# Performance work log

Measured on AMD Instinct MI355X. Metric: run time of the kernel, lower is better.

## Reference

```python
import jax, jax.numpy as jnp
import numpy as np

N, E = 4096, 131072
IN_DIM, HID, OUT_DIM = 128, 64, 128
H1 = 4                       # gat1 heads
D_MODEL = HID * H1           # 256
NHEAD = 4
D_FF = 2048


def setup_inputs() -> dict:
    key = jax.random.key(0)
    ks = jax.random.split(key, 16)
    def w(k, shape, scale=0.05):
        return jax.random.normal(k, shape, dtype=jnp.float32) * scale
    return {
        "x": jax.random.normal(ks[0], (N, IN_DIM), dtype=jnp.float32),
        "edge_index": jax.random.randint(ks[1], (2, E), 0, N, dtype=jnp.int32),
        "gat1_w": w(ks[2], (H1 * HID, IN_DIM)),
        "gat1_asrc": w(ks[3], (H1, HID)),
        "gat1_adst": w(ks[4], (H1, HID)),
        "gat1_b": jnp.zeros((H1 * HID,), jnp.float32),
        "in_proj_w": w(ks[5], (3 * D_MODEL, D_MODEL)),
        "in_proj_b": jnp.zeros((3 * D_MODEL,), jnp.float32),
        "out_proj_w": w(ks[6], (D_MODEL, D_MODEL)),
        "out_proj_b": jnp.zeros((D_MODEL,), jnp.float32),
        "lin1_w": w(ks[7], (D_FF, D_MODEL)),
        "lin1_b": jnp.zeros((D_FF,), jnp.float32),
        "lin2_w": w(ks[8], (D_MODEL, D_FF)),
        "lin2_b": jnp.zeros((D_MODEL,), jnp.float32),
        "ln1_g": jnp.ones((D_MODEL,), jnp.float32),
        "ln1_b": jnp.zeros((D_MODEL,), jnp.float32),
        "ln2_g": jnp.ones((D_MODEL,), jnp.float32),
        "ln2_b": jnp.zeros((D_MODEL,), jnp.float32),
        "gat2_w": w(ks[9], (OUT_DIM, D_MODEL)),
        "gat2_asrc": w(ks[10], (1, OUT_DIM)),
        "gat2_adst": w(ks[11], (1, OUT_DIM)),
        "gat2_b": jnp.zeros((OUT_DIM,), jnp.float32),
    }


def _add_self_loops(ei, n):
    loops = jnp.arange(n, dtype=ei.dtype)
    return jnp.concatenate([ei, jnp.stack([loops, loops])], axis=1)


def _segment_softmax(logits, seg, n):
    # numerically stable softmax over edges grouped by destination node
    m = jax.ops.segment_max(logits, seg, num_segments=n)
    m = jnp.where(jnp.isfinite(m), m, 0.0)
    e = jnp.exp(logits - m[seg])
    s = jax.ops.segment_sum(e, seg, num_segments=n)
    return e / (s[seg] + 1e-16)


def _gat(x, ei, W, asrc, adst, b, heads, out_ch):
    n = x.shape[0]
    h = (x @ W.T).reshape(n, heads, out_ch)          # [N,H,C]
    al_s = jnp.einsum('nhc,hc->nh', h, asrc)
    al_d = jnp.einsum('nhc,hc->nh', h, adst)
    src, dst = ei[0], ei[1]
    logits = jax.nn.leaky_relu(al_s[src] + al_d[dst], 0.2)   # [E,H]
    alpha = _segment_softmax(logits, dst, n)
    out = jax.ops.segment_sum(h[src] * alpha[:, :, None], dst, num_segments=n)
    return out.reshape(n, heads * out_ch) + b


def _ln(x, g, b):
    mu = x.mean(-1, keepdims=True)
    v = x.var(-1, keepdims=True)
    return (x - mu) / jnp.sqrt(v + 1e-5) * g + b


def _forward(x, edge_index, gat1_w, gat1_asrc, gat1_adst, gat1_b,
             in_proj_w, in_proj_b, out_proj_w, out_proj_b,
             lin1_w, lin1_b, lin2_w, lin2_b, ln1_g, ln1_b, ln2_g, ln2_b,
             gat2_w, gat2_asrc, gat2_adst, gat2_b):
    n = x.shape[0]
    ei = _add_self_loops(edge_index, n)
    h = jax.nn.elu(_gat(x, ei, gat1_w, gat1_asrc, gat1_adst, gat1_b, H1, HID))  # [N, 256]
    # TransformerEncoderLayer (post-norm, relu, no dropout in eval)
    hd = D_MODEL // NHEAD
    qkv = h @ in_proj_w.T + in_proj_b
    q, k, v = jnp.split(qkv, 3, axis=-1)
    q = q.reshape(n, NHEAD, hd)
    k = k.reshape(n, NHEAD, hd)
    v = v.reshape(n, NHEAD, hd)
    scores = jnp.einsum('qhd,khd->hqk', q, k) / jnp.sqrt(jnp.float32(hd))
    attn = jax.nn.softmax(scores, axis=-1)
    o = jnp.einsum('hqk,khd->qhd', attn, v).reshape(n, D_MODEL)
    o = o @ out_proj_w.T + out_proj_b
    h = _ln(h + o, ln1_g, ln1_b)
    ff = jax.nn.relu(h @ lin1_w.T + lin1_b) @ lin2_w.T + lin2_b
    h = _ln(h + ff, ln2_g, ln2_b)
    return _gat(h, ei, gat2_w, gat2_asrc, gat2_adst, gat2_b, 1, OUT_DIM)


def reference(x, edge_index, gat1_w, gat1_asrc, gat1_adst, gat1_b,
              in_proj_w, in_proj_b, out_proj_w, out_proj_b,
              lin1_w, lin1_b, lin2_w, lin2_b, ln1_g, ln1_b, ln2_g, ln2_b,
              gat2_w, gat2_asrc, gat2_adst, gat2_b):
    return _forward(x, edge_index, gat1_w, gat1_asrc, gat1_adst, gat1_b,
                    in_proj_w, in_proj_b, out_proj_w, out_proj_b,
                    lin1_w, lin1_b, lin2_w, lin2_b, ln1_g, ln1_b, ln2_g, ln2_b,
                    gat2_w, gat2_asrc, gat2_adst, gat2_b)
```

## Files before the change

kernel.cpp:

```cpp
#include <hip/hip_runtime.h>
#include <hip/hip_bf16.h>
#include <math.h>

#define NN 4096
#define NE 131072
#define EE (NE + NN)

typedef unsigned short u16;
typedef short s8v __attribute__((ext_vector_type(8)));
typedef float f4v __attribute__((ext_vector_type(4)));
typedef float f16v __attribute__((ext_vector_type(16)));

__device__ inline u16 f2b(float f) {
  __hip_bfloat16 h = __float2bfloat16(f);
  return __builtin_bit_cast(u16, h);
}
__device__ inline float b2f(u16 v) {
  unsigned int u = ((unsigned int)v) << 16;
  return __builtin_bit_cast(float, u);
}

__global__ void k_count(const int* __restrict__ ei, int* __restrict__ deg) {
  int e = blockIdx.x * 256 + threadIdx.x;
  if (e >= EE) return;
  int dst = (e < NE) ? ei[NE + e] : (e - NE);
  atomicAdd(&deg[dst], 1);
}

__global__ __launch_bounds__(1024) void k_scan(const int* __restrict__ deg, int* __restrict__ rowptr) {
  __shared__ int lds[1024];
  int t = threadIdx.x;
  int v0 = deg[t*4+0], v1 = deg[t*4+1], v2 = deg[t*4+2], v3 = deg[t*4+3];
  int s1 = v0+v1, s2 = s1+v2, s3 = s2+v3;
  lds[t] = s3;
  __syncthreads();
  for (int off = 1; off < 1024; off <<= 1) {
    int add = (t >= off) ? lds[t-off] : 0;
    __syncthreads();
    lds[t] += add;
    __syncthreads();
  }
  int base = lds[t] - s3;
  rowptr[t*4+1] = base + v0;
  rowptr[t*4+2] = base + s1;
  rowptr[t*4+3] = base + s2;
  rowptr[t*4+4] = base + s3;
  if (t == 0) rowptr[0] = 0;
}

__global__ void k_scatter(const int* __restrict__ ei, const int* __restrict__ rowptr,
                          int* __restrict__ cursor, int* __restrict__ csr_src) {
  int e = blockIdx.x * 256 + threadIdx.x;
  if (e >= EE) return;
  int src, dst;
  if (e < NE) { src = ei[e]; dst = ei[NE + e]; }
  else { src = e - NE; dst = src; }
  int pos = rowptr[dst] + atomicAdd(&cursor[dst], 1);
  csr_src[pos] = src;
}

__global__ __launch_bounds__(256) void k_f2b_all(
    const float* a0, u16* b0, int e0, const float* a1, u16* b1, int e1,
    const float* a2, u16* b2, int e2, const float* a3, u16* b3, int e3,
    const float* a4, u16* b4, int e4, const float* a5, u16* b5, int e5,
    const float* a6, u16* b6, int e6)
{
  int i = blockIdx.x * 256 + threadIdx.x;
  const float* s; u16* d; int base;
  if      (i < e0) { s=a0; d=b0; base=0;  }
  else if (i < e1) { s=a1; d=b1; base=e0; }
  else if (i < e2) { s=a2; d=b2; base=e1; }
  else if (i < e3) { s=a3; d=b3; base=e2; }
  else if (i < e4) { s=a4; d=b4; base=e3; }
  else if (i < e5) { s=a5; d=b5; base=e4; }
  else if (i < e6) { s=a6; d=b6; base=e5; }
  else return;
  int j = i - base;
  float4 v = ((const float4*)s)[j];
  u16 r[4] = {f2b(v.x), f2b(v.y), f2b(v.z), f2b(v.w)};
  *(uint2*)(d + (size_t)j*4) = *(uint2*)r;
}

template<int HEADS, int C>
__global__ __launch_bounds__(256) void k_alogits(
    const u16* __restrict__ featb, const float* __restrict__ asrc,
    const float* __restrict__ adst, float* __restrict__ als, float* __restrict__ ald)
{
  constexpr int F = HEADS * C;
  int n = blockIdx.x, t = threadIdx.x;
  float f = b2f(featb[(size_t)n*F + t]);
  float ps = f * asrc[t];
  float pd = f * adst[t];
  #pragma unroll
  for (int off = 32; off; off >>= 1) {
    ps += __shfl_xor(ps, off);
    pd += __shfl_xor(pd, off);
  }
  if constexpr (C == 64) {
    if ((t & 63) == 0) {
      int hh = t >> 6;
      als[(size_t)n*HEADS + hh] = ps;
      ald[(size_t)n*HEADS + hh] = pd;
    }
  } else {
    __shared__ float sh[2][2];
    if ((t & 63) == 0) { sh[t>>6][0] = ps; sh[t>>6][1] = pd; }
    __syncthreads();
    if (t == 0) {
      als[n] = sh[0][0] + sh[1][0];
      ald[n] = sh[0][1] + sh[1][1];
    }
  }
}

template<int HEADS, int C, bool DO_ELU, bool WB>
__global__ __launch_bounds__(256) void k_gat_agg(
    const u16* __restrict__ featb, const float* __restrict__ als,
    const float* __restrict__ ald, const float* __restrict__ bias,
    const int* __restrict__ rowptr, const int* __restrict__ csr_src,
    float* __restrict__ out, u16* __restrict__ outb)
{
  constexpr int F = HEADS * C;
  int n = blockIdx.x, t = threadIdx.x;
  __shared__ float m_sh[HEADS], s_sh[HEADS];
  __shared__ float alpha_sh[HEADS][64];
  __shared__ int src_sh[64];
  int start = rowptr[n];
  int deg = rowptr[n+1] - start;
  int lane = t & 63, wv = t >> 6;
  for (int hh = wv; hh < HEADS; hh += F/64) {
    float adl = ald[(size_t)n*HEADS + hh];
    float mx = -INFINITY;
    for (int i = lane; i < deg; i += 64) {
      int s = csr_src[start + i];
      float lg = als[(size_t)s*HEADS + hh] + adl;
      lg = (lg > 0.f) ? lg : 0.2f * lg;
      mx = fmaxf(mx, lg);
    }
    #pragma unroll
    for (int off = 32; off; off >>= 1) mx = fmaxf(mx, __shfl_xor(mx, off));
    float sm = 0.f;
    for (int i = lane; i < deg; i += 64) {
      int s = csr_src[start + i];
      float lg = als[(size_t)s*HEADS + hh] + adl;
      lg = (lg > 0.f) ? lg : 0.2f * lg;
      sm += expf(lg - mx);
    }
    #pragma unroll
    for (int off = 32; off; off >>= 1) sm += __shfl_xor(sm, off);
    if (lane == 0) { m_sh[hh] = mx; s_sh[hh] = sm; }
  }
  __syncthreads();
  int hh = t / C;
  int hh2 = t >> 6;
  int ia = t & 63;
  float acc0 = 0.f, acc1 = 0.f;
  for (int c0 = 0; c0 < deg; c0 += 64) {
    int cn = min(64, deg - c0);
    if (hh2 < HEADS && ia < cn) {
      int s = csr_src[start + c0 + ia];
      if (hh2 == 0) src_sh[ia] = s;
      float lg = als[(size_t)s*HEADS + hh2] + ald[(size_t)n*HEADS + hh2];
      lg = (lg > 0.f) ? lg : 0.2f * lg;
      alpha_sh[hh2][ia] = expf(lg - m_sh[hh2]);
    }
    __syncthreads();
    int i = 0;
    for (; i + 1 < cn; i += 2) {
      int s0 = src_sh[i], s1 = src_sh[i+1];
      float a0 = alpha_sh[hh][i], a1 = alpha_sh[hh][i+1];
      acc0 += a0 * b2f(featb[(size_t)s0*F + t]);
      acc1 += a1 * b2f(featb[(size_t)s1*F + t]);
    }
    if (i < cn)
      acc0 += alpha_sh[hh][i] * b2f(featb[(size_t)src_sh[i]*F + t]);
    __syncthreads();
  }
  float o = (acc0 + acc1) / (s_sh[hh] + 1e-16f) + bias[t];
  if (DO_ELU) o = (o > 0.f) ? o : (expf(o) - 1.f);
  out[(size_t)n*F + t] = o;
  if (WB) outb[(size_t)n*F + t] = f2b(o);
}

template<int MODE>
__global__ __launch_bounds__(256) void k_gemm_mfma(
    const u16* __restrict__ A, const u16* __restrict__ B,
    const float* __restrict__ bias, float* __restrict__ Cf, u16* __restrict__ Cb,
    u16* __restrict__ Qb, u16* __restrict__ Kb, u16* __restrict__ Vt,
    int M, int N, int K)
{
  __shared__ u16 Al[64*64];
  __shared__ u16 Bl[64*64];
  char* Ab = (char*)Al;
  char* Bb = (char*)Bl;
  const int t = threadIdx.x;
  const int lane = t & 63;
  const int lr = lane & 15, lk = lane >> 4;
  const int wid = t >> 6;
  const int wm = wid & 1, wn = wid >> 1;
  const int m0 = blockIdx.y * 64, n0 = blockIdx.x * 64;

  f4v acc[2][2];
  #pragma unroll
  for (int mi = 0; mi < 2; ++mi)
    #pragma unroll
    for (int ni = 0; ni < 2; ++ni)
      acc[mi][ni] = f4v{0.f, 0.f, 0.f, 0.f};

  for (int k0 = 0; k0 < K; k0 += 64) {
    #pragma unroll
    for (int i = 0; i < 2; ++i) {
      int idx = t + i*256;
      int row = idx >> 3, ch = idx & 7;
      s8v av = *(const s8v*)(A + (size_t)(m0 + row)*K + k0 + ch*8);
      *(s8v*)(Ab + row*128 + ((ch*16) ^ ((row & 7) << 4))) = av;
      s8v bv = *(const s8v*)(B + (size_t)(n0 + row)*K + k0 + ch*8);
      *(s8v*)(Bb + row*128 + ((ch*16) ^ ((row & 7) << 4))) = bv;
    }
    __syncthreads();
    #pragma unroll
    for (int ks = 0; ks < 2; ++ks) {
      s8v af[2], bfr[2];
      #pragma unroll
      for (int mi = 0; mi < 2; ++mi) {
        int row = wm*32 + mi*16 + lr;
        int ch = ks*4 + lk;
        af[mi] = *(const s8v*)(Ab + row*128 + ((ch*16) ^ ((row & 7) << 4)));
      }
      #pragma unroll
      for (int ni = 0; ni < 2; ++ni) {
        int row = wn*32 + ni*16 + lr;
        int ch = ks*4 + lk;
        bfr[ni] = *(const s8v*)(Bb + row*128 + ((ch*16) ^ ((row & 7) << 4)));
      }
      #pragma unroll
      for (int mi = 0; mi < 2; ++mi)
        #pragma unroll
        for (int ni = 0; ni < 2; ++ni)
          acc[mi][ni] = __builtin_amdgcn_mfma_f32_16x16x32_bf16(af[mi], bfr[ni], acc[mi][ni], 0, 0, 0);
    }
    __syncthreads();
  }
  #pragma unroll
  for (int ni = 0; ni < 2; ++ni) {
    int col = n0 + wn*32 + ni*16 + lr;
    float bc = bias ? bias[col] : 0.f;
    #pragma unroll
    for (int mi = 0; mi < 2; ++mi) {
      int row0 = m0 + wm*32 + mi*16 + lk*4;
      float v[4];
      #pragma unroll
      for (int r = 0; r < 4; ++r) v[r] = acc[mi][ni][r] + bc;
      if (MODE == 0) {
        #pragma unroll
        for (int r = 0; r < 4; ++r) Cf[(size_t)(row0 + r)*N + col] = v[r];
      } else if (MODE == 2) {
        #pragma unroll
        for (int r = 0; r < 4; ++r) Cb[(size_t)(row0 + r)*N + col] = f2b(v[r]);
      } else {
        if (col < 512) {
          int head = (col >> 6) & 3;
          int d = col & 63;
          u16* dst = ((col < 256) ? Qb : Kb) + (size_t)head*262144 + d;
          #pragma unroll
          for (int r = 0; r < 4; ++r) dst[(size_t)(row0 + r)*64] = f2b(v[r]);
        } else {
          int cc = col - 512;
          int head = cc >> 6;
          int d = cc & 63;
          int quad = row0 & 12;
          int qs = (quad == 4) ? 8 : ((quad == 8) ? 4 : quad);
          size_t nphys = (size_t)((row0 & ~15) | qs);
          u16 o4[4];
          #pragma unroll
          for (int r = 0; r < 4; ++r) o4[r] = f2b(v[r]);
          *(uint2*)(Vt + (size_t)head*262144 + (size_t)d*4096 + nphys) = *(uint2*)o4;
        }
      }
    }
  }
}

template<int MODE>
__global__ __launch_bounds__(256) void k_gemm2(
    const u16* __restrict__ A, const u16* __restrict__ B,
    const float* __restrict__ bias, float* __restrict__ Cf, u16* __restrict__ Cb,
    int M, int N, int K, int ksl)
{
  __shared__ u16 Al[128*64];
  __shared__ u16 Bl[64*64];
  char* Ab = (char*)Al;
  char* Bb = (char*)Bl;
  const int t = threadIdx.x;
  const int lane = t & 63;
  const int lr = lane & 15, lk = lane >> 4;
  const int wv = t >> 6;
  const int m0 = blockIdx.y * 128, n0 = blockIdx.x * 64;
  const int z = blockIdx.z;
  const int kbeg = z * ksl, kend = kbeg + ksl;

  f4v acc[2][4];
  #pragma unroll
  for (int mi = 0; mi < 2; ++mi)
    #pragma unroll
    for (int ni = 0; ni < 4; ++ni)
      acc[mi][ni] = f4v{0.f, 0.f, 0.f, 0.f};

  for (int k0 = kbeg; k0 < kend; k0 += 64) {
    #pragma unroll
    for (int i = 0; i < 4; ++i) {
      int idx = t + i*256;
      int row = idx >> 3, ch = idx & 7;
      s8v av = *(const s8v*)(A + (size_t)(m0 + row)*K + k0 + ch*8);
      *(s8v*)(Ab + row*128 + ((ch*16) ^ ((row & 7) << 4))) = av;
    }
    #pragma unroll
    for (int i = 0; i < 2; ++i) {
      int idx = t + i*256;
      int row = idx >> 3, ch = idx & 7;
      s8v bv = *(const s8v*)(B + (size_t)(n0 + row)*K + k0 + ch*8);
      *(s8v*)(Bb + row*128 + ((ch*16) ^ ((row & 7) << 4))) = bv;
    }
    __syncthreads();
    #pragma unroll
    for (int ks = 0; ks < 2; ++ks) {
      s8v af[2], bfr[4];
      #pragma unroll
      for (int mi = 0; mi < 2; ++mi) {
        int row = wv*32 + mi*16 + lr;
        int ch = ks*4 + lk;
        af[mi] = *(const s8v*)(Ab + row*128 + ((ch*16) ^ ((row & 7) << 4)));
      }
      #pragma unroll
      for (int ni = 0; ni < 4; ++ni) {
        int row = ni*16 + lr;
        int ch = ks*4 + lk;
        bfr[ni] = *(const s8v*)(Bb + row*128 + ((ch*16) ^ ((row & 7) << 4)));
      }
      #pragma unroll
      for (int mi = 0; mi < 2; ++mi)
        #pragma unroll
        for (int ni = 0; ni < 4; ++ni)
          acc[mi][ni] = __builtin_amdgcn_mfma_f32_16x16x32_bf16(af[mi], bfr[ni], acc[mi][ni], 0, 0, 0);
    }
    __syncthreads();
  }
  #pragma unroll
  for (int ni = 0; ni < 4; ++ni) {
    int col = n0 + ni*16 + lr;
    float bc = (MODE == 4) ? 0.f : bias[col];
    #pragma unroll
    for (int mi = 0; mi < 2; ++mi) {
      int row0 = m0 + wv*32 + mi*16 + lk*4;
      #pragma unroll
      for (int r = 0; r < 4; ++r) {
        float v = acc[mi][ni][r] + bc;
        if (MODE == 1) {
          v = fmaxf(v, 0.f);
          Cb[(size_t)(row0 + r)*N + col] = f2b(v);
        } else {
          (Cf + (size_t)z*M*N)[(size_t)(row0 + r)*N + col] = v;
        }
      }
    }
  }
}

template<bool WB>
__global__ __launch_bounds__(256) void k_ln(
    const float* __restrict__ a, const float* __restrict__ res,
    const float* __restrict__ g, const float* __restrict__ bb,
    float* __restrict__ out, u16* __restrict__ outb)
{
  int n = blockIdx.x, t = threadIdx.x;
  __shared__ float part[4];
  float v = a[(size_t)n*256 + t] + res[(size_t)n*256 + t];
  float s = v;
  #pragma unroll
  for (int off = 32; off; off >>= 1) s += __shfl_xor(s, off);
  if ((t & 63) == 0) part[t >> 6] = s;
  __syncthreads();
  float mean = (part[0] + part[1] + part[2] + part[3]) * (1.f/256.f);
  __syncthreads();
  float d = v - mean;
  float s2 = d * d;
  #pragma unroll
  for (int off = 32; off; off >>= 1) s2 += __shfl_xor(s2, off);
  if ((t & 63) == 0) part[t >> 6] = s2;
  __syncthreads();
  float var = (part[0] + part[1] + part[2] + part[3]) * (1.f/256.f);
  float rstd = rsqrtf(var + 1e-5f);
  float o = d * rstd * g[t] + bb[t];
  out[(size_t)n*256 + t] = o;
  if (WB) outb[(size_t)n*256 + t] = f2b(o);
}

template<bool WB>
__global__ __launch_bounds__(256) void k_ln_sk(
    const float* __restrict__ Po, const float* __restrict__ bias,
    const float* __restrict__ res, const float* __restrict__ g,
    const float* __restrict__ bb, float* __restrict__ out, u16* __restrict__ outb)
{
  int n = blockIdx.x, t = threadIdx.x;
  __shared__ float part[4];
  const size_t MN = (size_t)NN * 256;
  size_t idx = (size_t)n*256 + t;
  float v = Po[idx] + Po[MN + idx] + Po[2*MN + idx] + Po[3*MN + idx]
          + bias[t] + res[idx];
  float s = v;
  #pragma unroll
  for (int off = 32; off; off >>= 1) s += __shfl_xor(s, off);
  if ((t & 63) == 0) part[t >> 6] = s;
  __syncthreads();
  float mean = (part[0] + part[1] + part[2] + part[3]) * (1.f/256.f);
  __syncthreads();
  float d = v - mean;
  float s2 = d * d;
  #pragma unroll
  for (int off = 32; off; off >>= 1) s2 += __shfl_xor(s2, off);
  if ((t & 63) == 0) part[t >> 6] = s2;
  __syncthreads();
  float var = (part[0] + part[1] + part[2] + part[3]) * (1.f/256.f);
  float rstd = rsqrtf(var + 1e-5f);
  float o = d * rstd * g[t] + bb[t];
  out[idx] = o;
  if (WB) outb[idx] = f2b(o);
}

__global__ __launch_bounds__(256) void k_attn3(
    const u16* __restrict__ Qb, const u16* __restrict__ Kb,
    const u16* __restrict__ Vt, float* __restrict__ op0, float* __restrict__ op1,
    float* __restrict__ mball, float* __restrict__ lball)
{
  const int strip = blockIdx.x;
  const int head  = blockIdx.y;
  const int z     = blockIdx.z;
  const int t = threadIdx.x;
  const int wv = t >> 6;
  const int l = t & 63;
  const int lq = l & 31;
  const int lh = l >> 5;
  const int q0 = strip*128 + wv*32;

  __shared__ u16 Kl[64*64];
  __shared__ u16 Vl[64*64];
  char* Kc = (char*)Kl;
  char* Vc = (char*)Vl;

  const u16* Qh = Qb + (size_t)head * (4096*64);
  const u16* Kh = Kb + (size_t)head * (4096*64);
  const u16* Vh = Vt + (size_t)head * (64*4096);

  s8v qf[4];
#pragma unroll
  for (int dc = 0; dc < 4; ++dc)
    qf[dc] = *(const s8v*)(Qh + (size_t)(q0 + lq)*64 + dc*16 + lh*8);

  const int c0 = t, c1 = t + 256;
  const int kr0 = c0 >> 3, kc0 = c0 & 7;
  const int kr1 = c1 >> 3, kc1 = c1 & 7;
  const int kt0 = z * 512;
  const u16* gK0 = Kh + (size_t)(kt0 + kr0)*64 + kc0*8;
  const u16* gK1 = Kh + (size_t)(kt0 + kr1)*64 + kc1*8;
  const u16* gV0 = Vh + (size_t)kr0*4096 + kt0 + kc0*8;
  const u16* gV1 = Vh + (size_t)kr1*4096 + kt0 + kc1*8;
  const int lo0 = kr0*128 + ((kc0*16) ^ ((kr0 & 7) << 4));
  const int lo1 = kr1*128 + ((kc1*16) ^ ((kr1 & 7) << 4));

  {
    s8v a = *(const s8v*)gK0, b = *(const s8v*)gK1;
    s8v c = *(const s8v*)gV0, d = *(const s8v*)gV1;
    *(s8v*)(Kc + lo0) = a; *(s8v*)(Kc + lo1) = b;
    *(s8v*)(Vc + lo0) = c; *(s8v*)(Vc + lo1) = d;
  }
  __syncthreads();

  int roK[2][4];
#pragma unroll
  for (int c = 0; c < 2; ++c) {
    int row = c*32 + lq;
#pragma unroll
    for (int dc = 0; dc < 4; ++dc)
      roK[c][dc] = row*128 + ((dc*32 + lh*16) ^ ((row & 7) << 4));
  }
  int roV[2][2][2];
#pragma unroll
  for (int dm = 0; dm < 2; ++dm) {
    int row = dm*32 + lq;
#pragma unroll
    for (int c = 0; c < 2; ++c)
#pragma unroll
      for (int kc = 0; kc < 2; ++kc)
        roV[c][kc][dm] = row*128 + ((c*64 + kc*32 + lh*16) ^ ((row & 7) << 4));
  }

  f16v accO[2];
#pragma unroll
  for (int dm = 0; dm < 2; ++dm)
#pragma unroll
    for (int i = 0; i < 16; ++i) accO[dm][i] = 0.f;
  float mrow = -INFINITY, lrow = 0.f;
  const float CE = 0.18033688011112042f;

  s8v rK0, rK1, rV0, rV1;
  for (int tt = 0; tt < 8; ++tt) {
    if (tt < 7) {
      gK0 += 64*64; gK1 += 64*64; gV0 += 64; gV1 += 64;
      rK0 = *(const s8v*)gK0; rK1 = *(const s8v*)gK1;
      rV0 = *(const s8v*)gV0; rV1 = *(const s8v*)gV1;
    }
    s8v kf[2][4];
#pragma unroll
    for (int c = 0; c < 2; ++c)
#pragma unroll
      for (int dc = 0; dc < 4; ++dc)
        kf[c][dc] = *(const s8v*)(Kc + roK[c][dc]);
    f16v st[2];
#pragma unroll
    for (int c = 0; c < 2; ++c)
#pragma unroll
      for (int i = 0; i < 16; ++i) st[c][i] = 0.f;
#pragma unroll
    for (int dc = 0; dc < 4; ++dc) {
      st[0] = __builtin_amdgcn_mfma_f32_32x32x16_bf16(kf[0][dc], qf[dc], st[0], 0, 0, 0);
      st[1] = __builtin_amdgcn_mfma_f32_32x32x16_bf16(kf[1][dc], qf[dc], st[1], 0, 0, 0);
    }
    float mx = st[0][0];
#pragma unroll
    for (int i = 1; i < 16; ++i) mx = fmaxf(mx, st[0][i]);
#pragma unroll
    for (int i = 0; i < 16; ++i) mx = fmaxf(mx, st[1][i]);
    mx = fmaxf(mx, __shfl_xor(mx, 32));
    float mn = fmaxf(mrow, mx);
    float sc = exp2f((mrow - mn) * CE);
    mrow = mn;
    float ps = 0.f;
#pragma unroll
    for (int c = 0; c < 2; ++c)
#pragma unroll
      for (int i = 0; i < 16; ++i) {
        float p = exp2f((st[c][i] - mn) * CE);
        st[c][i] = p;
        ps += p;
      }
    ps += __shfl_xor(ps, 32);
    lrow = lrow * sc + ps;
#pragma unroll
    for (int dm = 0; dm < 2; ++dm)
#pragma unroll
      for (int i = 0; i < 16; ++i) accO[dm][i] *= sc;

#pragma unroll
    for (int c = 0; c < 2; ++c) {
#pragma unroll
      for (int kc = 0; kc < 2; ++kc) {
        s8v vf0 = *(const s8v*)(Vc + roV[c][kc][0]);
        s8v vf1 = *(const s8v*)(Vc + roV[c][kc][1]);
        union { s8v v; unsigned int w[4]; } pb;
#pragma unroll
        for (int wd = 0; wd < 4; ++wd) {
          u16 lo16 = f2b(st[c][kc*8 + wd*2]);
          u16 hi16 = f2b(st[c][kc*8 + wd*2 + 1]);
          pb.w[wd] = (unsigned int)lo16 | ((unsigned int)hi16 << 16);
        }
        accO[0] = __builtin_amdgcn_mfma_f32_32x32x16_bf16(vf0, pb.v, accO[0], 0, 0, 0);
        accO[1] = __builtin_amdgcn_mfma_f32_32x32x16_bf16(vf1, pb.v, accO[1], 0, 0, 0);
      }
    }
    __syncthreads();
    if (tt < 7) {
      *(s8v*)(Kc + lo0) = rK0; *(s8v*)(Kc + lo1) = rK1;
      *(s8v*)(Vc + lo0) = rV0; *(s8v*)(Vc + lo1) = rV1;
      __syncthreads();
    }
  }

  int q = q0 + lq;
  int pidx = (z*4 + head)*4096 + q;
  if (lh == 0) { mball[pidx] = mrow; lball[pidx] = lrow; }
  float* op = (z < 4) ? op0 : op1;
  size_t obase = ((size_t)((z & 3)*4 + head)*4096 + q)*64;
#pragma unroll
  for (int dm = 0; dm < 2; ++dm)
#pragma unroll
    for (int g = 0; g < 4; ++g) {
      f4v v;
#pragma unroll
      for (int rr = 0; rr < 4; ++rr) v[rr] = accO[dm][g*4 + rr];
      *(f4v*)&op[obase + dm*32 + lh*4 + g*8] = v;
    }
}

__global__ __launch_bounds__(256) void k_attn_mrg8(
    const float* __restrict__ op0, const float* __restrict__ op1,
    const float* __restrict__ mball, const float* __restrict__ lball,
    u16* __restrict__ attno_b)
{
  const int bq = blockIdx.x;
  const int head = blockIdx.y;
  const int t = threadIdx.x;
  const int q = bq*32 + (t >> 3);
  const int d0 = (t & 7) * 8;
  const float CE = 0.18033688011112042f;
  float m[8], M = -INFINITY;
#pragma unroll
  for (int z = 0; z < 8; ++z) {
    m[z] = mball[(z*4 + head)*4096 + q];
    M = fmaxf(M, m[z]);
  }
  float w[8], L = 0.f;
#pragma unroll
  for (int z = 0; z < 8; ++z) {
    w[z] = exp2f((m[z] - M) * CE);
    L += w[z] * lball[(z*4 + head)*4096 + q];
  }
  float inv = 1.f / L;
  float o[8] = {0,0,0,0,0,0,0,0};
#pragma unroll
  for (int z = 0; z < 8; ++z) {
    const float* op = (z < 4) ? op0 : op1;
    size_t base = ((size_t)((z & 3)*4 + head)*4096 + q)*64 + d0;
    f4v a = *(const f4v*)&op[base];
    f4v b = *(const f4v*)&op[base + 4];
#pragma unroll
    for (int i = 0; i < 4; ++i) { o[i] += w[z]*a[i]; o[4+i] += w[z]*b[i]; }
  }
  u16 o8[8];
#pragma unroll
  for (int i = 0; i < 8; ++i) o8[i] = f2b(o[i] * inv);
  *(uint4*)(attno_b + (size_t)q*256 + head*64 + d0) = *(uint4*)o8;
}

extern "C" void kernel_launch(void* const* d_in, const int* in_sizes, int n_in,
                              void* d_out, int out_size, void* d_ws, size_t ws_size,
                              hipStream_t stream)
{
  const float* x       = (const float*)d_in[0];
  const int*   ei      = (const int*)d_in[1];
  const float* gat1_w  = (const float*)d_in[2];
  const float* gat1_as = (const float*)d_in[3];
  const float* gat1_ad = (const float*)d_in[4];
  const float* gat1_b  = (const float*)d_in[5];
  const float* inp_w   = (const float*)d_in[6];
  const float* inp_b   = (const float*)d_in[7];
  const float* outp_w  = (const float*)d_in[8];
  const float* outp_b  = (const float*)d_in[9];
  const float* lin1_w  = (const float*)d_in[10];
  const float* lin1_b  = (const float*)d_in[11];
  const float* lin2_w  = (const float*)d_in[12];
  const float* lin2_b  = (const float*)d_in[13];
  const float* ln1_g   = (const float*)d_in[14];
  const float* ln1_bb  = (const float*)d_in[15];
  const float* ln2_g   = (const float*)d_in[16];
  const float* ln2_bb  = (const float*)d_in[17];
  const float* gat2_w  = (const float*)d_in[18];
  const float* gat2_as = (const float*)d_in[19];
  const float* gat2_ad = (const float*)d_in[20];
  const float* gat2_b  = (const float*)d_in[21];
  float* out = (float*)d_out;
  (void)in_sizes; (void)n_in; (void)out_size; (void)ws_size;

  char* ws = (char*)d_ws;
  size_t off = 0;
  auto nxt = [&](size_t bytes) { size_t r = off; off += (bytes + 255) & ~(size_t)255; return r; };
  int* deg      = (int*)(ws + nxt((size_t)NN*4));
  int* cursor   = (int*)(ws + nxt((size_t)NN*4));
  int* rowptr   = (int*)(ws + nxt((size_t)(NN+1)*4));
  int* csr_src  = (int*)(ws + nxt((size_t)EE*4));
  float* al1s   = (float*)(ws + nxt((size_t)NN*4*4));
  float* al1d   = (float*)(ws + nxt((size_t)NN*4*4));
  float* hgat1  = (float*)(ws + nxt((size_t)NN*256*4));
  float* tmp256 = (float*)(ws + nxt((size_t)NN*256*4));
  float* hln1   = (float*)(ws + nxt((size_t)NN*256*4));
  float* hln2   = (float*)(ws + nxt((size_t)NN*256*4));
  float* Po     = (float*)(ws + nxt((size_t)4*NN*256*4));
  float* al2s   = (float*)(ws + nxt((size_t)NN*4));
  float* al2d   = (float*)(ws + nxt((size_t)NN*4));
  float* mball  = (float*)(ws + nxt((size_t)32*NN*4));
  float* lball  = (float*)(ws + nxt((size_t)32*NN*4));
  u16* x_b      = (u16*)(ws + nxt((size_t)NN*128*2));
  u16* feat1_b  = (u16*)(ws + nxt((size_t)NN*256*2));
  u16* feat2_b  = (u16*)(ws + nxt((size_t)NN*128*2));
  u16* hgat1_b  = (u16*)(ws + nxt((size_t)NN*256*2));
  u16* attno_b  = (u16*)(ws + nxt((size_t)NN*256*2));
  u16* hln1_b   = (u16*)(ws + nxt((size_t)NN*256*2));
  u16* hln2_b   = (u16*)(ws + nxt((size_t)NN*256*2));
  u16* ff1_b    = (u16*)(ws + nxt((size_t)NN*2048*2));
  u16* Qb       = (u16*)(ws + nxt((size_t)4*4096*64*2));
  u16* Kb       = (u16*)(ws + nxt((size_t)4*4096*64*2));
  u16* Vt       = (u16*)(ws + nxt((size_t)4*4096*64*2));
  u16* inp_w_b  = (u16*)(ws + nxt((size_t)768*256*2));
  u16* outp_w_b = (u16*)(ws + nxt((size_t)256*256*2));
  u16* lin1_w_b = (u16*)(ws + nxt((size_t)2048*256*2));
  u16* lin2_w_b = (u16*)(ws + nxt((size_t)256*2048*2));
  u16* gat1_w_b = (u16*)(ws + nxt((size_t)256*128*2));
  u16* gat2_w_b = (u16*)(ws + nxt((size_t)128*256*2));

  float* op0 = Po;
  float* op1 = (float*)ff1_b;

  hipMemsetAsync(deg, 0, (size_t)NN*4, stream);
  hipMemsetAsync(cursor, 0, (size_t)NN*4, stream);
  k_count<<<(EE+255)/256, 256, 0, stream>>>(ei, deg);
  k_scan<<<1, 1024, 0, stream>>>(deg, rowptr);
  k_scatter<<<(EE+255)/256, 256, 0, stream>>>(ei, rowptr, cursor, csr_src);

  k_f2b_all<<<1856, 256, 0, stream>>>(
      inp_w,  inp_w_b,  49152,
      outp_w, outp_w_b, 65536,
      lin1_w, lin1_w_b, 196608,
      lin2_w, lin2_w_b, 327680,
      gat1_w, gat1_w_b, 335872,
      gat2_w, gat2_w_b, 344064,
      x,      x_b,      475136);

  k_gemm_mfma<2><<<dim3(4, 64), 256, 0, stream>>>(x_b, gat1_w_b, nullptr, nullptr, feat1_b, nullptr, nullptr, nullptr, NN, 256, 128);
  k_alogits<4,64><<<NN, 256, 0, stream>>>(feat1_b, gat1_as, gat1_ad, al1s, al1d);
  k_gat_agg<4,64,true,true><<<NN, 256, 0, stream>>>(feat1_b, al1s, al1d, gat1_b, rowptr, csr_src, hgat1, hgat1_b);

  k_gemm_mfma<3><<<dim3(12, 64), 256, 0, stream>>>(hgat1_b, inp_w_b, inp_b, nullptr, nullptr, Qb, Kb, Vt, NN, 768, 256);
  k_attn3<<<dim3(32, 4, 8), 256, 0, stream>>>(Qb, Kb, Vt, op0, op1, mball, lball);
  k_attn_mrg8<<<dim3(128, 4), 256, 0, stream>>>(op0, op1, mball, lball, attno_b);
  k_gemm_mfma<0><<<dim3(4, 64), 256, 0, stream>>>(attno_b, outp_w_b, outp_b, tmp256, nullptr, nullptr, nullptr, nullptr, NN, 256, 256);
  k_ln<true><<<NN, 256, 0, stream>>>(tmp256, hgat1, ln1_g, ln1_bb, hln1, hln1_b);
  k_gemm2<1><<<dim3(32, 32), 256, 0, stream>>>(hln1_b, lin1_w_b, lin1_b, nullptr, ff1_b, NN, 2048, 256, 256);
  k_gemm2<4><<<dim3(4, 32, 4), 256, 0, stream>>>(ff1_b, lin2_w_b, nullptr, Po, nullptr, NN, 256, 2048, 512);
  k_ln_sk<true><<<NN, 256, 0, stream>>>(Po, lin2_b, hln1, ln2_g, ln2_bb, hln2, hln2_b);

  k_gemm_mfma<2><<<dim3(2, 64), 256, 0, stream>>>(hln2_b, gat2_w_b, nullptr, nullptr, feat2_b, nullptr, nullptr, nullptr, NN, 128, 256);
  k_alogits<1,128><<<NN, 128, 0, stream>>>(feat2_b, gat2_as, gat2_ad, al2s, al2d);
  k_gat_agg<1,128,false,false><<<NN, 128, 0, stream>>>(feat2_b, al2s, al2d, gat2_b, rowptr, csr_src, out, nullptr);
}
```

Measured before the change: 275.0 us.

## Double-buffer attention K/V tiles, halve key splits, unroll GAT aggregation by four

The attention kernel now double-buffers its K/V tiles in LDS, so it needs one barrier per tile instead of two. It also halves the number of key splits (4 instead of 8, 1024 keys each), which halves the partial outputs written and merged, at the cost of fewer blocks in flight. GAT aggregation unrolls its edge loop by four with separate accumulators to increase the number of gathers in flight. The P-matrix bf16 conversion switches to a manual round-to-nearest-even bit trick, which does not handle NaN the way the library conversion does.

```diff
diff --git a/kernel.cpp b/kernel.cpp
--- a/kernel.cpp
+++ b/kernel.cpp
@@ -14,6 +14,11 @@
 __device__ inline u16 f2b(float f) {
   __hip_bfloat16 h = __float2bfloat16(f);
   return __builtin_bit_cast(u16, h);
+}
+__device__ inline u16 f2bf(float f) {
+  unsigned int b = __builtin_bit_cast(unsigned int, f);
+  b += 0x7FFFu + ((b >> 16) & 1u);
+  return (u16)(b >> 16);
 }
 __device__ inline float b2f(u16 v) {
   unsigned int u = ((unsigned int)v) << 16;
@@ -154,7 +159,7 @@
   int hh = t / C;
   int hh2 = t >> 6;
   int ia = t & 63;
-  float acc0 = 0.f, acc1 = 0.f;
+  float acc0 = 0.f, acc1 = 0.f, acc2 = 0.f, acc3 = 0.f;
   for (int c0 = 0; c0 < deg; c0 += 64) {
     int cn = min(64, deg - c0);
     if (hh2 < HEADS && ia < cn) {
@@ -166,17 +171,18 @@
     }
     __syncthreads();
     int i = 0;
-    for (; i + 1 < cn; i += 2) {
-      int s0 = src_sh[i], s1 = src_sh[i+1];
-      float a0 = alpha_sh[hh][i], a1 = alpha_sh[hh][i+1];
-      acc0 += a0 * b2f(featb[(size_t)s0*F + t]);
-      acc1 += a1 * b2f(featb[(size_t)s1*F + t]);
-    }
-    if (i < cn)
+    for (; i + 3 < cn; i += 4) {
+      int s0 = src_sh[i], s1 = src_sh[i+1], s2 = src_sh[i+2], s3 = src_sh[i+3];
+      acc0 += alpha_sh[hh][i]   * b2f(featb[(size_t)s0*F + t]);
+      acc1 += alpha_sh[hh][i+1] * b2f(featb[(size_t)s1*F + t]);
+      acc2 += alpha_sh[hh][i+2] * b2f(featb[(size_t)s2*F + t]);
+      acc3 += alpha_sh[hh][i+3] * b2f(featb[(size_t)s3*F + t]);
+    }
+    for (; i < cn; ++i)
       acc0 += alpha_sh[hh][i] * b2f(featb[(size_t)src_sh[i]*F + t]);
     __syncthreads();
   }
-  float o = (acc0 + acc1) / (s_sh[hh] + 1e-16f) + bias[t];
+  float o = ((acc0 + acc1) + (acc2 + acc3)) / (s_sh[hh] + 1e-16f) + bias[t];
   if (DO_ELU) o = (o > 0.f) ? o : (expf(o) - 1.f);
   out[(size_t)n*F + t] = o;
   if (WB) outb[(size_t)n*F + t] = f2b(o);
@@ -429,7 +435,7 @@
 
 __global__ __launch_bounds__(256) void k_attn3(
     const u16* __restrict__ Qb, const u16* __restrict__ Kb,
-    const u16* __restrict__ Vt, float* __restrict__ op0, float* __restrict__ op1,
+    const u16* __restrict__ Vt, float* __restrict__ op,
     float* __restrict__ mball, float* __restrict__ lball)
 {
   const int strip = blockIdx.x;
@@ -442,10 +448,8 @@
   const int lh = l >> 5;
   const int q0 = strip*128 + wv*32;
 
-  __shared__ u16 Kl[64*64];
-  __shared__ u16 Vl[64*64];
-  char* Kc = (char*)Kl;
-  char* Vc = (char*)Vl;
+  __shared__ u16 Kl[2][64*64];
+  __shared__ u16 Vl[2][64*64];
 
   const u16* Qh = Qb + (size_t)head * (4096*64);
   const u16* Kh = Kb + (size_t)head * (4096*64);
@@ -459,7 +463,7 @@
   const int c0 = t, c1 = t + 256;
   const int kr0 = c0 >> 3, kc0 = c0 & 7;
   const int kr1 = c1 >> 3, kc1 = c1 & 7;
-  const int kt0 = z * 512;
+  const int kt0 = z * 1024;
   const u16* gK0 = Kh + (size_t)(kt0 + kr0)*64 + kc0*8;
   const u16* gK1 = Kh + (size_t)(kt0 + kr1)*64 + kc1*8;
   const u16* gV0 = Vh + (size_t)kr0*4096 + kt0 + kc0*8;
@@ -470,8 +474,8 @@
   {
     s8v a = *(const s8v*)gK0, b = *(const s8v*)gK1;
     s8v c = *(const s8v*)gV0, d = *(const s8v*)gV1;
-    *(s8v*)(Kc + lo0) = a; *(s8v*)(Kc + lo1) = b;
-    *(s8v*)(Vc + lo0) = c; *(s8v*)(Vc + lo1) = d;
+    *(s8v*)((char*)Kl[0] + lo0) = a; *(s8v*)((char*)Kl[0] + lo1) = b;
+    *(s8v*)((char*)Vl[0] + lo0) = c; *(s8v*)((char*)Vl[0] + lo1) = d;
   }
   __syncthreads();
 
@@ -503,8 +507,13 @@
   const float CE = 0.18033688011112042f;
 
   s8v rK0, rK1, rV0, rV1;
-  for (int tt = 0; tt < 8; ++tt) {
-    if (tt < 7) {
+  for (int tt = 0; tt < 16; ++tt) {
+    const int cur = tt & 1;
+    char* Kc = (char*)Kl[cur];
+    char* Vc = (char*)Vl[cur];
+    char* Kn = (char*)Kl[cur ^ 1];
+    char* Vn = (char*)Vl[cur ^ 1];
+    if (tt < 15) {
       gK0 += 64*64; gK1 += 64*64; gV0 += 64; gV1 += 64;
       rK0 = *(const s8v*)gK0; rK1 = *(const s8v*)gK1;
       rV0 = *(const s8v*)gV0; rV1 = *(const s8v*)gV1;
@@ -559,27 +568,24 @@
         union { s8v v; unsigned int w[4]; } pb;
 #pragma unroll
         for (int wd = 0; wd < 4; ++wd) {
-          u16 lo16 = f2b(st[c][kc*8 + wd*2]);
-          u16 hi16 = f2b(st[c][kc*8 + wd*2 + 1]);
-          pb.w[wd] = (unsigned int)lo16 | ((unsigned int)hi16 << 16);
+          pb.w[wd] = (unsigned int)f2bf(st[c][kc*8 + wd*2])
+                   | ((unsigned int)f2bf(st[c][kc*8 + wd*2 + 1]) << 16);
         }
         accO[0] = __builtin_amdgcn_mfma_f32_32x32x16_bf16(vf0, pb.v, accO[0], 0, 0, 0);
         accO[1] = __builtin_amdgcn_mfma_f32_32x32x16_bf16(vf1, pb.v, accO[1], 0, 0, 0);
       }
     }
-    __syncthreads();
-    if (tt < 7) {
-      *(s8v*)(Kc + lo0) = rK0; *(s8v*)(Kc + lo1) = rK1;
-      *(s8v*)(Vc + lo0) = rV0; *(s8v*)(Vc + lo1) = rV1;
-      __syncthreads();
-    }
+    if (tt < 15) {
+      *(s8v*)(Kn + lo0) = rK0; *(s8v*)(Kn + lo1) = rK1;
+      *(s8v*)(Vn + lo0) = rV0; *(s8v*)(Vn + lo1) = rV1;
+    }
+    __syncthreads();
   }
 
   int q = q0 + lq;
   int pidx = (z*4 + head)*4096 + q;
   if (lh == 0) { mball[pidx] = mrow; lball[pidx] = lrow; }
-  float* op = (z < 4) ? op0 : op1;
-  size_t obase = ((size_t)((z & 3)*4 + head)*4096 + q)*64;
+  size_t obase = ((size_t)(z*4 + head)*4096 + q)*64;
 #pragma unroll
   for (int dm = 0; dm < 2; ++dm)
 #pragma unroll
@@ -591,10 +597,9 @@
     }
 }
 
-__global__ __launch_bounds__(256) void k_attn_mrg8(
-    const float* __restrict__ op0, const float* __restrict__ op1,
-    const float* __restrict__ mball, const float* __restrict__ lball,
-    u16* __restrict__ attno_b)
+__global__ __launch_bounds__(256) void k_attn_mrg4(
+    const float* __restrict__ op, const float* __restrict__ mball,
+    const float* __restrict__ lball, u16* __restrict__ attno_b)
 {
   const int bq = blockIdx.x;
   const int head = blockIdx.y;
@@ -602,24 +607,23 @@
   const int q = bq*32 + (t >> 3);
   const int d0 = (t & 7) * 8;
   const float CE = 0.18033688011112042f;
-  float m[8], M = -INFINITY;
-#pragma unroll
-  for (int z = 0; z < 8; ++z) {
+  float m[4], M = -INFINITY;
+#pragma unroll
+  for (int z = 0; z < 4; ++z) {
     m[z] = mball[(z*4 + head)*4096 + q];
     M = fmaxf(M, m[z]);
   }
-  float w[8], L = 0.f;
-#pragma unroll
-  for (int z = 0; z < 8; ++z) {
+  float w[4], L = 0.f;
+#pragma unroll
+  for (int z = 0; z < 4; ++z) {
     w[z] = exp2f((m[z] - M) * CE);
     L += w[z] * lball[(z*4 + head)*4096 + q];
   }
   float inv = 1.f / L;
   float o[8] = {0,0,0,0,0,0,0,0};
 #pragma unroll
-  for (int z = 0; z < 8; ++z) {
-    const float* op = (z < 4) ? op0 : op1;
-    size_t base = ((size_t)((z & 3)*4 + head)*4096 + q)*64 + d0;
+  for (int z = 0; z < 4; ++z) {
+    size_t base = ((size_t)(z*4 + head)*4096 + q)*64 + d0;
     f4v a = *(const f4v*)&op[base];
     f4v b = *(const f4v*)&op[base + 4];
 #pragma unroll
@@ -676,8 +680,8 @@
   float* Po     = (float*)(ws + nxt((size_t)4*NN*256*4));
   float* al2s   = (float*)(ws + nxt((size_t)NN*4));
   float* al2d   = (float*)(ws + nxt((size_t)NN*4));
-  float* mball  = (float*)(ws + nxt((size_t)32*NN*4));
-  float* lball  = (float*)(ws + nxt((size_t)32*NN*4));
+  float* mball  = (float*)(ws + nxt((size_t)16*NN*4));
+  float* lball  = (float*)(ws + nxt((size_t)16*NN*4));
   u16* x_b      = (u16*)(ws + nxt((size_t)NN*128*2));
   u16* feat1_b  = (u16*)(ws + nxt((size_t)NN*256*2));
   u16* feat2_b  = (u16*)(ws + nxt((size_t)NN*128*2));
@@ -696,9 +700,6 @@
   u16* gat1_w_b = (u16*)(ws + nxt((size_t)256*128*2));
   u16* gat2_w_b = (u16*)(ws + nxt((size_t)128*256*2));
 
-  float* op0 = Po;
-  float* op1 = (float*)ff1_b;
-
   hipMemsetAsync(deg, 0, (size_t)NN*4, stream);
   hipMemsetAsync(cursor, 0, (size_t)NN*4, stream);
   k_count<<<(EE+255)/256, 256, 0, stream>>>(ei, deg);
@@ -719,8 +720,8 @@
   k_gat_agg<4,64,true,true><<<NN, 256, 0, stream>>>(feat1_b, al1s, al1d, gat1_b, rowptr, csr_src, hgat1, hgat1_b);
 
   k_gemm_mfma<3><<<dim3(12, 64), 256, 0, stream>>>(hgat1_b, inp_w_b, inp_b, nullptr, nullptr, Qb, Kb, Vt, NN, 768, 256);
-  k_attn3<<<dim3(32, 4, 8), 256, 0, stream>>>(Qb, Kb, Vt, op0, op1, mball, lball);
-  k_attn_mrg8<<<dim3(128, 4), 256, 0, stream>>>(op0, op1, mball, lball, attno_b);
+  k_attn3<<<dim3(32, 4, 4), 256, 0, stream>>>(Qb, Kb, Vt, Po, mball, lball);
+  k_attn_mrg4<<<dim3(128, 4), 256, 0, stream>>>(Po, mball, lball, attno_b);
   k_gemm_mfma<0><<<dim3(4, 64), 256, 0, stream>>>(attno_b, outp_w_b, outp_b, tmp256, nullptr, nullptr, nullptr, nullptr, NN, 256, 256);
   k_ln<true><<<NN, 256, 0, stream>>>(tmp256, hgat1, ln1_g, ln1_bb, hln1, hln1_b);
   k_gemm2<1><<<dim3(32, 32), 256, 0, stream>>>(hln1_b, lin1_w_b, lin1_b, nullptr, ff1_b, NN, 2048, 256, 256);
```

Result: faster. 266.0 us (-3.3%).
